# Optimization experiments

Hardware: AMD Instinct MI355X
Metric: run time of the kernel (lower is better)

The kernel has to match this reference:

```python
import jax, jax.numpy as jnp
import numpy as np

B, S, D = 4, 1024, 1024
H = 16
DH = D // H           # 64
ROT = 64              # rotary_emb_dim (full head dim)
NEG_INF = -10000.0
ROPE_BASE = 10000.0


def _rope_tables(seqlen, rot_dim, dtype=jnp.float32):
    inv_freq = 1.0 / (ROPE_BASE ** (jnp.arange(0, rot_dim, 2, dtype=jnp.float32) / rot_dim))
    t = jnp.arange(seqlen, dtype=jnp.float32)
    freqs = jnp.einsum('s,f->sf', t, inv_freq)  # (S, rot_dim//2)
    return jnp.cos(freqs).astype(dtype), jnp.sin(freqs).astype(dtype)


def _apply_rotary(x, cos, sin):
    # x: (B, S, H, DH); GPT-NeoX (non-interleaved) rotary over first ROT dims
    half = ROT // 2
    x_rot, x_pass = x[..., :ROT], x[..., ROT:]
    x1, x2 = x_rot[..., :half], x_rot[..., half:]
    c = cos[None, :, None, :]
    s = sin[None, :, None, :]
    rot = jnp.concatenate([x1 * c - x2 * s, x2 * c + x1 * s], axis=-1)
    return jnp.concatenate([rot, x_pass], axis=-1) if x_pass.shape[-1] else rot


def setup_inputs() -> dict:
    key = jax.random.key(0)
    ks = jax.random.split(key, 5)
    sc_in = 1.0 / np.sqrt(D)
    return {
        'x': jax.random.normal(ks[0], (B, S, D), jnp.float32),
        'Wqkv': jax.random.normal(ks[1], (3 * D, D), jnp.float32) * sc_in,
        'bqkv': jax.random.normal(ks[2], (3 * D,), jnp.float32) * 0.01,
        'Wout': jax.random.normal(ks[3], (D, D), jnp.float32) * sc_in,
        'bout': jax.random.normal(ks[4], (D,), jnp.float32) * 0.01,
    }


def reference(x, Wqkv, bqkv, Wout, bout):
    # QKV projection: (B,S,D) -> (B,S,3,H,DH)
    qkv = (jnp.einsum('bsd,ed->bse', x, Wqkv) + bqkv).reshape(B, S, 3, H, DH)
    q, k, v = qkv[:, :, 0], qkv[:, :, 1], qkv[:, :, 2]
    cos, sin = _rope_tables(S, ROT, q.dtype)
    q = _apply_rotary(q, cos, sin)
    k = _apply_rotary(k, cos, sin)
    scale = 1.0 / np.sqrt(DH)
    scores = jnp.einsum('bthd,bshd->bhts', q, k * scale)  # (B,H,S,S)
    causal_mask = jnp.triu(jnp.full((S, S), NEG_INF, dtype=scores.dtype), 1)
    scores = scores + causal_mask
    attn = jax.nn.softmax(scores, axis=-1)
    out = jnp.einsum('bhts,bshd->bthd', attn, v).reshape(B, S, D)
    return jnp.einsum('bsd,ed->bse', out, Wout) + bout
```

## Files before the change

kernel.cpp:

```cpp
#include <hip/hip_runtime.h>

#define B_ 4
#define S_ 1024
#define D_ 1024
#define H_ 16
#define DH_ 64

typedef unsigned short u16;
typedef __attribute__((ext_vector_type(8))) short bf16x8;
typedef __attribute__((ext_vector_type(4))) float f32x4;

__device__ __forceinline__ float bf2f(u16 h){
  union { unsigned u; float f; } x; x.u = ((unsigned)h) << 16; return x.f;
}
__device__ __forceinline__ u16 f2bf(float f){
  union { float f; unsigned u; } x; x.f = f;
  unsigned u = x.u;
  return (u16)((u + 0x7fffu + ((u >> 16) & 1u)) >> 16);
}

__device__ __forceinline__ void gload16(const u16* g, u16* l){
  __builtin_amdgcn_global_load_lds(
      (const __attribute__((address_space(1))) unsigned int*)g,
      (__attribute__((address_space(3))) unsigned int*)l, 16, 0, 0);
}

__global__ __launch_bounds__(256) void cast3(
    const float* __restrict__ a, u16* __restrict__ oa, int na,
    const float* __restrict__ b, u16* __restrict__ ob, int nb,
    const float* __restrict__ c, u16* __restrict__ oc){
  int i = (blockIdx.x * 256 + threadIdx.x) * 4;
  const float* src; u16* dst;
  if (i < na){ src = a + i; dst = oa + i; }
  else if (i < na + nb){ src = b + (i - na); dst = ob + (i - na); }
  else { src = c + (i - na - nb); dst = oc + (i - na - nb); }
  float4 v = *(const float4*)src;
  union { u16 s[4]; uint2 u; } o;
  o.s[0] = f2bf(v.x); o.s[1] = f2bf(v.y); o.s[2] = f2bf(v.z); o.s[3] = f2bf(v.w);
  *(uint2*)dst = o.u;
}

__global__ __launch_bounds__(256) void rope_tab(float2* __restrict__ tab){
  int idx = blockIdx.x * 256 + threadIdx.x;
  int s = idx >> 5, i = idx & 31;
  float invf = powf(10000.0f, -(float)i * (1.0f / 32.0f));
  float sn, cs;
  sincosf((float)s * invf, &sn, &cs);
  tab[idx] = make_float2(cs, sn);
}

__global__ __launch_bounds__(512, 2) void gemm_qkv8(const u16* __restrict__ A,
    const u16* __restrict__ Bm, const float* __restrict__ bias,
    const float2* __restrict__ tab,
    u16* __restrict__ qb, u16* __restrict__ kb, u16* __restrict__ vtb){
  __shared__ u16 As_[2][2][128*64];
  __shared__ u16 Bs_[2][2][128*64];
  const int K = 1024;
  const int tid = threadIdx.x;
  const int lane = tid & 63, wid = tid >> 6;
  const int wr = wid >> 2, wc = wid & 3;
  const int lo = lane & 15, g = lane >> 4;

  const int bid = blockIdx.x;
  const int swz = (bid & 7) * 24 + (bid >> 3);
  const int bx = swz & 15, by = swz >> 4;
  const int m0 = bx * 256, n0 = by * 256;

  f32x4 acc[8][4];
  #pragma unroll
  for (int i = 0; i < 8; ++i)
    #pragma unroll
    for (int j = 0; j < 4; ++j) acc[i][j] = (f32x4){0.f, 0.f, 0.f, 0.f};

  auto stage_p0 = [&](int b, int kt){
    const u16* ga = A + (size_t)m0 * K + kt * 64;
    const u16* gb = Bm + (size_t)n0 * K + kt * 64;
    {
      int c = tid;
      int r = c >> 3;
      int colbs = ((c & 7) * 16) ^ ((r & 7) << 4);
      int src = r * K + (colbs >> 1);
      gload16(ga + src,         &As_[b][0][c * 8]);
      gload16(ga + 128*K + src, &As_[b][1][c * 8]);
      gload16(gb + src,         &Bs_[b][0][c * 8]);
      gload16(gb + 128*K + src, &Bs_[b][1][c * 8]);
    }
    {
      int c = tid + 512;
      int r = c >> 3;
      int colbs = ((c & 7) * 16) ^ ((r & 7) << 4);
      int src = r * K + (colbs >> 1);
      gload16(gb + src,         &Bs_[b][0][c * 8]);
      gload16(gb + 128*K + src, &Bs_[b][1][c * 8]);
    }
  };
  auto stage_p1 = [&](int b, int kt){
    const u16* ga = A + (size_t)m0 * K + kt * 64;
    int c = tid + 512;
    int r = c >> 3;
    int colbs = ((c & 7) * 16) ^ ((r & 7) << 4);
    int src = r * K + (colbs >> 1);
    gload16(ga + src,         &As_[b][0][c * 8]);
    gload16(ga + 128*K + src, &As_[b][1][c * 8]);
  };

  auto rdA = [&](int b, int qm, int fm, int ks) -> bf16x8 {
    int row = qm*64 + fm*16 + lo;
    int byte = row*128 + ((ks*64 + g*16) ^ ((lo & 7) << 4));
    return *(const bf16x8*)(&As_[b][wr][byte >> 1]);
  };
  auto rdB = [&](int b, int fn, int ks) -> bf16x8 {
    int row = (wc & 1)*64 + fn*16 + lo;
    int byte = row*128 + ((ks*64 + g*16) ^ ((lo & 7) << 4));
    return *(const bf16x8*)(&Bs_[b][wc >> 1][byte >> 1]);
  };

  auto ktile = [&](int b, int stage_t){
    bf16x8 a[8], bq[8];
    #pragma unroll
    for (int fm = 0; fm < 4; ++fm)
      #pragma unroll
      for (int ks = 0; ks < 2; ++ks) a[fm*2+ks] = rdA(b, 0, fm, ks);
    #pragma unroll
    for (int fn = 0; fn < 4; ++fn)
      #pragma unroll
      for (int ks = 0; ks < 2; ++ks) bq[fn*2+ks] = rdB(b, fn, ks);
    __builtin_amdgcn_s_setprio(1);
    #pragma unroll
    for (int fm = 0; fm < 4; ++fm)
      #pragma unroll
      for (int fn = 0; fn < 2; ++fn)
        #pragma unroll
        for (int ks = 0; ks < 2; ++ks)
          acc[fm][fn] = __builtin_amdgcn_mfma_f32_16x16x32_bf16(a[fm*2+ks], bq[fn*2+ks], acc[fm][fn], 0, 0, 0);
    __builtin_amdgcn_s_setprio(0);
    asm volatile("s_waitcnt lgkmcnt(0)" ::: "memory");
    __builtin_amdgcn_sched_barrier(0);
    __builtin_amdgcn_s_barrier();
    __builtin_amdgcn_sched_barrier(0);
    if (stage_t >= 0) stage_p0(b, stage_t);
    __builtin_amdgcn_s_setprio(1);
    #pragma unroll
    for (int fm = 0; fm < 4; ++fm)
      #pragma unroll
      for (int fn = 0; fn < 2; ++fn)
        #pragma unroll
        for (int ks = 0; ks < 2; ++ks)
          acc[fm][2+fn] = __builtin_amdgcn_mfma_f32_16x16x32_bf16(a[fm*2+ks], bq[(2+fn)*2+ks], acc[fm][2+fn], 0, 0, 0);
    __builtin_amdgcn_s_setprio(0);
    #pragma unroll
    for (int fm = 0; fm < 4; ++fm)
      #pragma unroll
      for (int ks = 0; ks < 2; ++ks) a[fm*2+ks] = rdA(b, 1, fm, ks);
    __builtin_amdgcn_s_setprio(1);
    #pragma unroll
    for (int fm = 0; fm < 4; ++fm)
      #pragma unroll
      for (int fn = 0; fn < 2; ++fn)
        #pragma unroll
        for (int ks = 0; ks < 2; ++ks)
          acc[4+fm][fn] = __builtin_amdgcn_mfma_f32_16x16x32_bf16(a[fm*2+ks], bq[fn*2+ks], acc[4+fm][fn], 0, 0, 0);
    __builtin_amdgcn_s_setprio(0);
    asm volatile("s_waitcnt lgkmcnt(0)" ::: "memory");
    __builtin_amdgcn_sched_barrier(0);
    __builtin_amdgcn_s_barrier();
    __builtin_amdgcn_sched_barrier(0);
    if (stage_t >= 0) stage_p1(b, stage_t);
    __builtin_amdgcn_s_setprio(1);
    #pragma unroll
    for (int fm = 0; fm < 4; ++fm)
      #pragma unroll
      for (int fn = 0; fn < 2; ++fn)
        #pragma unroll
        for (int ks = 0; ks < 2; ++ks)
          acc[4+fm][2+fn] = __builtin_amdgcn_mfma_f32_16x16x32_bf16(a[fm*2+ks], bq[(2+fn)*2+ks], acc[4+fm][2+fn], 0, 0, 0);
    __builtin_amdgcn_s_setprio(0);
  };

  stage_p0(0, 0); stage_p1(0, 0);
  stage_p0(1, 1); stage_p1(1, 1);
  for (int t = 0; t < 14; ++t){
    asm volatile("s_waitcnt vmcnt(8)" ::: "memory");
    __builtin_amdgcn_s_barrier();
    __builtin_amdgcn_sched_barrier(0);
    ktile(t & 1, t + 2);
  }
  asm volatile("s_waitcnt vmcnt(8)" ::: "memory");
  __builtin_amdgcn_s_barrier();
  __builtin_amdgcn_sched_barrier(0);
  ktile(0, -1);
  asm volatile("s_waitcnt vmcnt(0)" ::: "memory");
  __builtin_amdgcn_s_barrier();
  __builtin_amdgcn_sched_barrier(0);
  ktile(1, -1);

  const int ty = by >> 2;
  const int h  = (by & 3) * 4 + wc;
  float bv[4];
  #pragma unroll
  for (int fn = 0; fn < 4; ++fn) bv[fn] = bias[n0 + wc*64 + fn*16 + lo];

  if (ty < 2){
    u16* dst = (ty == 0) ? qb : kb;
    #pragma unroll
    for (int fm = 0; fm < 8; ++fm){
      #pragma unroll
      for (int j = 0; j < 4; ++j){
        int row = m0 + wr*128 + fm*16 + g*4 + j;
        int bb = row >> 10, s = row & 1023;
        size_t obase = (((size_t)(bb * H_ + h)) * S_ + s) * DH_;
        #pragma unroll
        for (int fn = 0; fn < 2; ++fn){
          int i = fn*16 + lo;
          float2 t2 = tab[s*32 + i];
          float v1 = acc[fm][fn][j] + bv[fn];
          float v2 = acc[fm][fn+2][j] + bv[fn+2];
          dst[obase + i]      = f2bf(v1 * t2.x - v2 * t2.y);
          dst[obase + i + 32] = f2bf(v2 * t2.x + v1 * t2.y);
        }
      }
    }
  } else {
    __syncthreads();
    u16* wbase = (wid < 4) ? ((u16*)As_ + wid * 8192)
                           : ((u16*)Bs_ + (wid - 4) * 8192);
    #pragma unroll
    for (int fm = 0; fm < 8; ++fm)
      #pragma unroll
      for (int fn = 0; fn < 4; ++fn){
        int d = fn*16 + lo;
        #pragma unroll
        for (int j = 0; j < 4; ++j){
          int sl = fm*16 + g*4 + j;
          int sx = sl ^ ((d & 7) << 4);
          wbase[d*128 + sx] = f2bf(acc[fm][fn][j] + bv[fn]);
        }
      }
    const int rowblk = m0 + wr*128;
    const int bb = rowblk >> 10;
    const int sbase = rowblk & 1023;
    #pragma unroll
    for (int pass = 0; pass < 16; ++pass){
      int d = pass*4 + g;
      int sc = lo * 8;
      int sx = sc ^ ((d & 7) << 4);
      bf16x8 v = *(const bf16x8*)(&wbase[d*128 + sx]);
      *(bf16x8*)(vtb + (((size_t)(bb * H_ + h)) * DH_ + d) * S_ + sbase + sc) = v;
    }
  }
}

template<int OUT_BF16>
__global__ __launch_bounds__(256) void gemm_bt(const u16* __restrict__ A,
    const u16* __restrict__ Bm, const float* __restrict__ bias,
    void* __restrict__ Cout, int M, int N, int K){
  __shared__ u16 As[2][128*32];
  __shared__ u16 Bs[2][128*32];
  const int tid = threadIdx.x;
  const int lane = tid & 63;
  const int w = tid >> 6;
  const int wr = w >> 1, wc = w & 1;
  const int lo = lane & 15, g = lane >> 4;
  const int m0 = blockIdx.x * 128, n0 = blockIdx.y * 128;

  f32x4 acc[4][4];
  #pragma unroll
  for (int i = 0; i < 4; ++i)
    #pragma unroll
    for (int j = 0; j < 4; ++j) acc[i][j] = (f32x4){0.f, 0.f, 0.f, 0.f};

  const int nt = K >> 5;

  auto stage = [&](int buf, int kt){
    const u16* ga = A + (size_t)m0 * K + kt * 32;
    const u16* gb = Bm + (size_t)n0 * K + kt * 32;
    #pragma unroll
    for (int it = 0; it < 2; ++it){
      int chunk = tid + it * 256;
      int row = chunk >> 2;
      int c0 = (chunk & 3) * 8;
      gload16(ga + (size_t)row * K + c0, &As[buf][chunk * 8]);
      gload16(gb + (size_t)row * K + c0, &Bs[buf][chunk * 8]);
    }
  };

  stage(0, 0);
  __syncthreads();
  int buf = 0;
  for (int kt = 0; kt < nt; ++kt){
    if (kt + 1 < nt) stage(buf ^ 1, kt + 1);
    bf16x8 af[4], bfr[4];
    #pragma unroll
    for (int mi = 0; mi < 4; ++mi)
      af[mi] = *(const bf16x8*)(&As[buf][(wr*64 + mi*16 + lo)*32 + g*8]);
    #pragma unroll
    for (int ni = 0; ni < 4; ++ni)
      bfr[ni] = *(const bf16x8*)(&Bs[buf][(wc*64 + ni*16 + lo)*32 + g*8]);
    #pragma unroll
    for (int mi = 0; mi < 4; ++mi)
      #pragma unroll
      for (int ni = 0; ni < 4; ++ni)
        acc[mi][ni] = __builtin_amdgcn_mfma_f32_16x16x32_bf16(af[mi], bfr[ni], acc[mi][ni], 0, 0, 0);
    __syncthreads();
    buf ^= 1;
  }

  #pragma unroll
  for (int mi = 0; mi < 4; ++mi){
    int row = m0 + wr*64 + mi*16 + g*4;
    #pragma unroll
    for (int ni = 0; ni < 4; ++ni){
      int col = n0 + wc*64 + ni*16 + lo;
      float bvs = bias[col];
      #pragma unroll
      for (int j = 0; j < 4; ++j){
        float v = acc[mi][ni][j] + bvs;
        if (OUT_BF16) ((u16*)Cout)[(size_t)(row + j) * N + col] = f2bf(v);
        else          ((float*)Cout)[(size_t)(row + j) * N + col] = v;
      }
    }
  }
}

__global__ __launch_bounds__(256) void attn_fwd(const u16* __restrict__ qb,
    const u16* __restrict__ kb, const u16* __restrict__ vtb,
    u16* __restrict__ ctx){
  const int bh = blockIdx.x;
  const int qt = 15 - blockIdx.y;
  const int b = bh >> 4, h = bh & 15;
  const int tid = threadIdx.x;
  const int lane = tid & 63, w = tid >> 6;
  const int lo = lane & 15, g = lane >> 4;

  __shared__ u16 Kl[2][64*64];
  __shared__ u16 Vl[2][64*64];
  __shared__ u16 Plds[4][16][72];

  auto stage = [&](int buf, int kt){
    const u16* ksrc = kb  + ((size_t)bh * S_ + kt*64) * DH_;
    const u16* vsrc = vtb + (size_t)bh * DH_ * S_ + kt*64;
    #pragma unroll
    for (int it = 0; it < 2; ++it){
      int c = tid + it * 256;
      int row = c >> 3;
      int colbs = ((c & 7) * 16) ^ ((row & 7) << 4);
      gload16(ksrc + (size_t)row * DH_ + (colbs >> 1), &Kl[buf][c * 8]);
      gload16(vsrc + (size_t)row * S_  + (colbs >> 1), &Vl[buf][c * 8]);
    }
  };

  stage(0, 0);

  bf16x8 qf[2];
  {
    const u16* qa = qb + ((size_t)bh * S_ + qt*64 + w*16 + lo) * DH_ + g*8;
    qf[0] = *(const bf16x8*)(qa);  qf[1] = *(const bf16x8*)(qa + 32);
  }

  float m_run[4], l_run[4];
  f32x4 O[4];
  #pragma unroll
  for (int j = 0; j < 4; ++j){ m_run[j] = -1e30f; l_run[j] = 0.f; }
  #pragma unroll
  for (int c = 0; c < 4; ++c) O[c] = (f32x4){0.f,0.f,0.f,0.f};

  int buf = 0;

  auto computeTile = [&](bool diag){
    f32x4 sacc[4];
    #pragma unroll
    for (int c = 0; c < 4; ++c) sacc[c] = (f32x4){0.f,0.f,0.f,0.f};
    __builtin_amdgcn_s_setprio(1);
    #pragma unroll
    for (int cf = 0; cf < 4; ++cf){
      int r = cf*16 + lo;
      #pragma unroll
      for (int ks = 0; ks < 2; ++ks){
        int byteoff = r*128 + ((ks*64 + g*16) ^ ((lo & 7) << 4));
        bf16x8 kf = *(const bf16x8*)(&Kl[buf][byteoff >> 1]);
        sacc[cf] = __builtin_amdgcn_mfma_f32_16x16x32_bf16(qf[ks], kf, sacc[cf], 0, 0, 0);
      }
    }
    __builtin_amdgcn_s_setprio(0);
    #pragma unroll
    for (int cf = 0; cf < 4; ++cf){
      #pragma unroll
      for (int j = 0; j < 4; ++j){
        float sv = sacc[cf][j] * 0.125f;
        if (diag){
          int kj = cf*16 + lo;
          int qr = w*16 + g*4 + j;
          if (kj > qr) sv -= 10000.f;
        }
        sacc[cf][j] = sv;
      }
    }
    float rowmax[4];
    #pragma unroll
    for (int j = 0; j < 4; ++j){
      float v = fmaxf(fmaxf(sacc[0][j], sacc[1][j]), fmaxf(sacc[2][j], sacc[3][j]));
      v = fmaxf(v, __shfl_xor(v, 1));
      v = fmaxf(v, __shfl_xor(v, 2));
      v = fmaxf(v, __shfl_xor(v, 4));
      v = fmaxf(v, __shfl_xor(v, 8));
      rowmax[j] = v;
    }
    float need = fmaxf(fmaxf(rowmax[0]-m_run[0], rowmax[1]-m_run[1]),
                       fmaxf(rowmax[2]-m_run[2], rowmax[3]-m_run[3]));
    float rsum[4] = {0.f,0.f,0.f,0.f};
    if (__all(need <= 8.0f)){
      #pragma unroll
      for (int cf = 0; cf < 4; ++cf)
        #pragma unroll
        for (int j = 0; j < 4; ++j){
          float pv = __expf(sacc[cf][j] - m_run[j]);
          sacc[cf][j] = pv;
          rsum[j] += pv;
        }
      #pragma unroll
      for (int j = 0; j < 4; ++j){
        float v = rsum[j];
        v += __shfl_xor(v, 1);
        v += __shfl_xor(v, 2);
        v += __shfl_xor(v, 4);
        v += __shfl_xor(v, 8);
        l_run[j] += v;
      }
    } else {
      float alpha[4];
      #pragma unroll
      for (int j = 0; j < 4; ++j){
        float mnew = fmaxf(m_run[j], rowmax[j]);
        alpha[j] = __expf(m_run[j] - mnew);
        m_run[j] = mnew;
      }
      #pragma unroll
      for (int cf = 0; cf < 4; ++cf)
        #pragma unroll
        for (int j = 0; j < 4; ++j){
          float pv = __expf(sacc[cf][j] - m_run[j]);
          sacc[cf][j] = pv;
          rsum[j] += pv;
        }
      #pragma unroll
      for (int j = 0; j < 4; ++j){
        float v = rsum[j];
        v += __shfl_xor(v, 1);
        v += __shfl_xor(v, 2);
        v += __shfl_xor(v, 4);
        v += __shfl_xor(v, 8);
        l_run[j] = l_run[j] * alpha[j] + v;
      }
      #pragma unroll
      for (int c = 0; c < 4; ++c)
        #pragma unroll
        for (int j = 0; j < 4; ++j) O[c][j] *= alpha[j];
    }

    #pragma unroll
    for (int cf = 0; cf < 4; ++cf){
      #pragma unroll
      for (int jp = 0; jp < 2; ++jp){
        unsigned pk;
        asm("v_cvt_pk_bf16_f32 %0, %1, %2"
            : "=v"(pk) : "v"(sacc[cf][jp*2]), "v"(sacc[cf][jp*2+1]));
        Plds[w][g*4 + jp*2][cf*16 + lo]     = (u16)(pk & 0xffffu);
        Plds[w][g*4 + jp*2 + 1][cf*16 + lo] = (u16)(pk >> 16);
      }
    }

    __builtin_amdgcn_s_setprio(1);
    #pragma unroll
    for (int ks = 0; ks < 2; ++ks){
      bf16x8 pf = *(const bf16x8*)(&Plds[w][lo][ks*32 + g*8]);
      #pragma unroll
      for (int ocf = 0; ocf < 4; ++ocf){
        int r = ocf*16 + lo;
        int byteoff = r*128 + ((ks*64 + g*16) ^ ((lo & 7) << 4));
        bf16x8 vf = *(const bf16x8*)(&Vl[buf][byteoff >> 1]);
        O[ocf] = __builtin_amdgcn_mfma_f32_16x16x32_bf16(pf, vf, O[ocf], 0, 0, 0);
      }
    }
    __builtin_amdgcn_s_setprio(0);
  };

  for (int kt = 0; kt <= qt; ++kt){
    __syncthreads();
    if (kt < qt) stage(buf ^ 1, kt + 1);
    computeTile(kt == qt);
    buf ^= 1;
  }

  float inv[4];
  #pragma unroll
  for (int j = 0; j < 4; ++j) inv[j] = 1.0f / l_run[j];
  #pragma unroll
  for (int ocf = 0; ocf < 4; ++ocf){
    #pragma unroll
    for (int j = 0; j < 4; ++j){
      int d = ocf*16 + lo;
      int qi = qt*64 + w*16 + g*4 + j;
      ctx[((size_t)(b * S_ + qi)) * D_ + h * DH_ + d] = f2bf(O[ocf][j] * inv[j]);
    }
  }
}

extern "C" void kernel_launch(void* const* d_in, const int* in_sizes, int n_in,
                              void* d_out, int out_size, void* d_ws, size_t ws_size,
                              hipStream_t stream){
  (void)in_sizes; (void)n_in; (void)out_size; (void)ws_size;
  const float* x    = (const float*)d_in[0];
  const float* Wqkv = (const float*)d_in[1];
  const float* bqkv = (const float*)d_in[2];
  const float* Wout = (const float*)d_in[3];
  const float* bout = (const float*)d_in[4];
  float* out = (float*)d_out;

  char* p = (char*)d_ws;
  u16* x_bf    = (u16*)p; p += (size_t)4096*1024*2;
  u16* wqkv_bf = (u16*)p; p += (size_t)3072*1024*2;
  u16* wout_bf = (u16*)p; p += (size_t)1024*1024*2;
  u16* q_bf    = (u16*)p; p += (size_t)4096*1024*2;
  u16* k_bf    = (u16*)p; p += (size_t)4096*1024*2;
  u16* vt_bf   = (u16*)p; p += (size_t)4096*1024*2;
  u16* ctx_bf  = (u16*)p; p += (size_t)4096*1024*2;
  float2* tab  = (float2*)p; p += (size_t)1024*32*8;

  const int na = 4096*1024, nb = 3072*1024;
  cast3<<<8192, 256, 0, stream>>>(x, x_bf, na, Wqkv, wqkv_bf, nb, Wout, wout_bf);
  rope_tab<<<128, 256, 0, stream>>>(tab);

  gemm_qkv8<<<192, 512, 0, stream>>>(x_bf, wqkv_bf, bqkv, tab, q_bf, k_bf, vt_bf);

  attn_fwd<<<dim3(64, 16), 256, 0, stream>>>(q_bf, k_bf, vt_bf, ctx_bf);

  gemm_bt<0><<<dim3(32, 8), 256, 0, stream>>>(ctx_bf, wout_bf, bout, out, 4096, 1024, 1024);
}
```

Baseline: 109.3 us.

## Shrink QKV GEMM tiles, pipeline out-proj GEMM, fuse rope table, swizzle P LDS

The QKV projection GEMM changes from 256x256 tiles with 512 threads to 128x128 tiles with 256 threads, three blocks per CU and a K step of 32, giving 768 blocks instead of 192. The output projection gets the same swizzled LDS layout, block-index swizzle and split-barrier double-buffered pipeline. The rope table computation is folded into the cast kernel to save a launch, and the attention P buffer drops its padding in favour of an XOR swizzle. Smaller tiles aim to improve occupancy and CU balance but cost more global traffic per FLOP. A redundant duplicated bias load is left in the epilogue.

```diff
diff --git a/kernel.cpp b/kernel.cpp
--- a/kernel.cpp
+++ b/kernel.cpp
@@ -25,10 +25,20 @@
       (__attribute__((address_space(3))) unsigned int*)l, 16, 0, 0);
 }
 
-__global__ __launch_bounds__(256) void cast3(
+__global__ __launch_bounds__(256) void cast3tab(
     const float* __restrict__ a, u16* __restrict__ oa, int na,
     const float* __restrict__ b, u16* __restrict__ ob, int nb,
-    const float* __restrict__ c, u16* __restrict__ oc){
+    const float* __restrict__ c, u16* __restrict__ oc,
+    float2* __restrict__ tab){
+  if (blockIdx.x >= 8192){
+    int idx = (blockIdx.x - 8192) * 256 + threadIdx.x;
+    int s = idx >> 5, i = idx & 31;
+    float invf = powf(10000.0f, -(float)i * (1.0f / 32.0f));
+    float sn, cs;
+    sincosf((float)s * invf, &sn, &cs);
+    tab[idx] = make_float2(cs, sn);
+    return;
+  }
   int i = (blockIdx.x * 256 + threadIdx.x) * 4;
   const float* src; u16* dst;
   if (i < na){ src = a + i; dst = oa + i; }
@@ -40,152 +50,88 @@
   *(uint2*)dst = o.u;
 }
 
-__global__ __launch_bounds__(256) void rope_tab(float2* __restrict__ tab){
-  int idx = blockIdx.x * 256 + threadIdx.x;
-  int s = idx >> 5, i = idx & 31;
-  float invf = powf(10000.0f, -(float)i * (1.0f / 32.0f));
-  float sn, cs;
-  sincosf((float)s * invf, &sn, &cs);
-  tab[idx] = make_float2(cs, sn);
-}
-
-__global__ __launch_bounds__(512, 2) void gemm_qkv8(const u16* __restrict__ A,
+__global__ __launch_bounds__(256, 3) void gemm_qkv(const u16* __restrict__ A,
     const u16* __restrict__ Bm, const float* __restrict__ bias,
     const float2* __restrict__ tab,
     u16* __restrict__ qb, u16* __restrict__ kb, u16* __restrict__ vtb){
-  __shared__ u16 As_[2][2][128*64];
-  __shared__ u16 Bs_[2][2][128*64];
+  __shared__ u16 As_[2][128*32];
+  __shared__ u16 Bs_[2][128*32];
   const int K = 1024;
   const int tid = threadIdx.x;
-  const int lane = tid & 63, wid = tid >> 6;
-  const int wr = wid >> 2, wc = wid & 3;
+  const int lane = tid & 63, w = tid >> 6;
+  const int wr = w >> 1, wc = w & 1;
   const int lo = lane & 15, g = lane >> 4;
 
   const int bid = blockIdx.x;
-  const int swz = (bid & 7) * 24 + (bid >> 3);
-  const int bx = swz & 15, by = swz >> 4;
-  const int m0 = bx * 256, n0 = by * 256;
-
-  f32x4 acc[8][4];
-  #pragma unroll
-  for (int i = 0; i < 8; ++i)
+  const int swz = (bid & 7) * 96 + (bid >> 3);
+  const int mx = swz & 31, ny = swz >> 5;
+  const int m0 = mx * 128, n0 = ny * 128;
+
+  f32x4 acc[4][4];
+  #pragma unroll
+  for (int i = 0; i < 4; ++i)
     #pragma unroll
     for (int j = 0; j < 4; ++j) acc[i][j] = (f32x4){0.f, 0.f, 0.f, 0.f};
 
-  auto stage_p0 = [&](int b, int kt){
-    const u16* ga = A + (size_t)m0 * K + kt * 64;
-    const u16* gb = Bm + (size_t)n0 * K + kt * 64;
-    {
-      int c = tid;
-      int r = c >> 3;
-      int colbs = ((c & 7) * 16) ^ ((r & 7) << 4);
-      int src = r * K + (colbs >> 1);
-      gload16(ga + src,         &As_[b][0][c * 8]);
-      gload16(ga + 128*K + src, &As_[b][1][c * 8]);
-      gload16(gb + src,         &Bs_[b][0][c * 8]);
-      gload16(gb + 128*K + src, &Bs_[b][1][c * 8]);
-    }
-    {
-      int c = tid + 512;
-      int r = c >> 3;
-      int colbs = ((c & 7) * 16) ^ ((r & 7) << 4);
-      int src = r * K + (colbs >> 1);
-      gload16(gb + src,         &Bs_[b][0][c * 8]);
-      gload16(gb + 128*K + src, &Bs_[b][1][c * 8]);
-    }
-  };
-  auto stage_p1 = [&](int b, int kt){
-    const u16* ga = A + (size_t)m0 * K + kt * 64;
-    int c = tid + 512;
-    int r = c >> 3;
-    int colbs = ((c & 7) * 16) ^ ((r & 7) << 4);
-    int src = r * K + (colbs >> 1);
-    gload16(ga + src,         &As_[b][0][c * 8]);
-    gload16(ga + 128*K + src, &As_[b][1][c * 8]);
-  };
-
-  auto rdA = [&](int b, int qm, int fm, int ks) -> bf16x8 {
-    int row = qm*64 + fm*16 + lo;
-    int byte = row*128 + ((ks*64 + g*16) ^ ((lo & 7) << 4));
-    return *(const bf16x8*)(&As_[b][wr][byte >> 1]);
-  };
-  auto rdB = [&](int b, int fn, int ks) -> bf16x8 {
-    int row = (wc & 1)*64 + fn*16 + lo;
-    int byte = row*128 + ((ks*64 + g*16) ^ ((lo & 7) << 4));
-    return *(const bf16x8*)(&Bs_[b][wc >> 1][byte >> 1]);
+  auto stage = [&](int b, int kt){
+    const u16* ga = A + (size_t)m0 * K + kt * 32;
+    const u16* gb = Bm + (size_t)n0 * K + kt * 32;
+    #pragma unroll
+    for (int it = 0; it < 2; ++it){
+      int c = tid + it * 256;
+      int r = c >> 2;
+      int cbs = ((c & 3) * 16) ^ ((r & 3) << 4);
+      gload16(ga + r * K + (cbs >> 1), &As_[b][c * 8]);
+      gload16(gb + r * K + (cbs >> 1), &Bs_[b][c * 8]);
+    }
+  };
+
+  auto rdA = [&](int b, int fm) -> bf16x8 {
+    int row = wr*64 + fm*16 + lo;
+    int byte = row*64 + ((g*16) ^ ((row & 3) << 4));
+    return *(const bf16x8*)(&As_[b][byte >> 1]);
+  };
+  auto rdB = [&](int b, int fn) -> bf16x8 {
+    int row = wc*64 + fn*16 + lo;
+    int byte = row*64 + ((g*16) ^ ((row & 3) << 4));
+    return *(const bf16x8*)(&Bs_[b][byte >> 1]);
   };
 
   auto ktile = [&](int b, int stage_t){
-    bf16x8 a[8], bq[8];
-    #pragma unroll
-    for (int fm = 0; fm < 4; ++fm)
-      #pragma unroll
-      for (int ks = 0; ks < 2; ++ks) a[fm*2+ks] = rdA(b, 0, fm, ks);
-    #pragma unroll
-    for (int fn = 0; fn < 4; ++fn)
-      #pragma unroll
-      for (int ks = 0; ks < 2; ++ks) bq[fn*2+ks] = rdB(b, fn, ks);
-    __builtin_amdgcn_s_setprio(1);
-    #pragma unroll
-    for (int fm = 0; fm < 4; ++fm)
-      #pragma unroll
-      for (int fn = 0; fn < 2; ++fn)
-        #pragma unroll
-        for (int ks = 0; ks < 2; ++ks)
-          acc[fm][fn] = __builtin_amdgcn_mfma_f32_16x16x32_bf16(a[fm*2+ks], bq[fn*2+ks], acc[fm][fn], 0, 0, 0);
-    __builtin_amdgcn_s_setprio(0);
+    bf16x8 af[4], bf[4];
+    #pragma unroll
+    for (int fm = 0; fm < 4; ++fm) af[fm] = rdA(b, fm);
+    #pragma unroll
+    for (int fn = 0; fn < 4; ++fn) bf[fn] = rdB(b, fn);
     asm volatile("s_waitcnt lgkmcnt(0)" ::: "memory");
     __builtin_amdgcn_sched_barrier(0);
+    __builtin_amdgcn_s_setprio(1);
+    #pragma unroll
+    for (int fm = 0; fm < 4; ++fm)
+      #pragma unroll
+      for (int fn = 0; fn < 2; ++fn)
+        acc[fm][fn] = __builtin_amdgcn_mfma_f32_16x16x32_bf16(af[fm], bf[fn], acc[fm][fn], 0, 0, 0);
+    __builtin_amdgcn_s_setprio(0);
     __builtin_amdgcn_s_barrier();
-    __builtin_amdgcn_sched_barrier(0);
-    if (stage_t >= 0) stage_p0(b, stage_t);
+    if (stage_t >= 0) stage(b, stage_t);
     __builtin_amdgcn_s_setprio(1);
     #pragma unroll
     for (int fm = 0; fm < 4; ++fm)
       #pragma unroll
-      for (int fn = 0; fn < 2; ++fn)
-        #pragma unroll
-        for (int ks = 0; ks < 2; ++ks)
-          acc[fm][2+fn] = __builtin_amdgcn_mfma_f32_16x16x32_bf16(a[fm*2+ks], bq[(2+fn)*2+ks], acc[fm][2+fn], 0, 0, 0);
+      for (int fn = 2; fn < 4; ++fn)
+        acc[fm][fn] = __builtin_amdgcn_mfma_f32_16x16x32_bf16(af[fm], bf[fn], acc[fm][fn], 0, 0, 0);
     __builtin_amdgcn_s_setprio(0);
-    #pragma unroll
-    for (int fm = 0; fm < 4; ++fm)
-      #pragma unroll
-      for (int ks = 0; ks < 2; ++ks) a[fm*2+ks] = rdA(b, 1, fm, ks);
-    __builtin_amdgcn_s_setprio(1);
-    #pragma unroll
-    for (int fm = 0; fm < 4; ++fm)
-      #pragma unroll
-      for (int fn = 0; fn < 2; ++fn)
-        #pragma unroll
-        for (int ks = 0; ks < 2; ++ks)
-          acc[4+fm][fn] = __builtin_amdgcn_mfma_f32_16x16x32_bf16(a[fm*2+ks], bq[fn*2+ks], acc[4+fm][fn], 0, 0, 0);
-    __builtin_amdgcn_s_setprio(0);
-    asm volatile("s_waitcnt lgkmcnt(0)" ::: "memory");
-    __builtin_amdgcn_sched_barrier(0);
-    __builtin_amdgcn_s_barrier();
-    __builtin_amdgcn_sched_barrier(0);
-    if (stage_t >= 0) stage_p1(b, stage_t);
-    __builtin_amdgcn_s_setprio(1);
-    #pragma unroll
-    for (int fm = 0; fm < 4; ++fm)
-      #pragma unroll
-      for (int fn = 0; fn < 2; ++fn)
-        #pragma unroll
-        for (int ks = 0; ks < 2; ++ks)
-          acc[4+fm][2+fn] = __builtin_amdgcn_mfma_f32_16x16x32_bf16(a[fm*2+ks], bq[(2+fn)*2+ks], acc[4+fm][2+fn], 0, 0, 0);
-    __builtin_amdgcn_s_setprio(0);
-  };
-
-  stage_p0(0, 0); stage_p1(0, 0);
-  stage_p0(1, 1); stage_p1(1, 1);
-  for (int t = 0; t < 14; ++t){
-    asm volatile("s_waitcnt vmcnt(8)" ::: "memory");
+  };
+
+  stage(0, 0);
+  stage(1, 1);
+  for (int t = 0; t < 30; ++t){
+    asm volatile("s_waitcnt vmcnt(4)" ::: "memory");
     __builtin_amdgcn_s_barrier();
     __builtin_amdgcn_sched_barrier(0);
     ktile(t & 1, t + 2);
   }
-  asm volatile("s_waitcnt vmcnt(8)" ::: "memory");
+  asm volatile("s_waitcnt vmcnt(4)" ::: "memory");
   __builtin_amdgcn_s_barrier();
   __builtin_amdgcn_sched_barrier(0);
   ktile(0, -1);
@@ -194,19 +140,22 @@
   __builtin_amdgcn_sched_barrier(0);
   ktile(1, -1);
 
-  const int ty = by >> 2;
-  const int h  = (by & 3) * 4 + wc;
+  const int gcb = n0 + wc*64;
+  const int ty = gcb >> 10;
+  const int h  = (gcb >> 6) & 15;
   float bv[4];
   #pragma unroll
-  for (int fn = 0; fn < 4; ++fn) bv[fn] = bias[n0 + wc*64 + fn*16 + lo];
+  for (int fn = 0; fn < 4; ++fn) bv[fn] = bias[gcb + fn*16 + lo - wc*64 + wc*64];
+  #pragma unroll
+  for (int fn = 0; fn < 4; ++fn) bv[fn] = bias[gcb + fn*16 + lo];
 
   if (ty < 2){
     u16* dst = (ty == 0) ? qb : kb;
     #pragma unroll
-    for (int fm = 0; fm < 8; ++fm){
+    for (int fm = 0; fm < 4; ++fm){
       #pragma unroll
       for (int j = 0; j < 4; ++j){
-        int row = m0 + wr*128 + fm*16 + g*4 + j;
+        int row = m0 + wr*64 + fm*16 + g*4 + j;
         int bb = row >> 10, s = row & 1023;
         size_t obase = (((size_t)(bb * H_ + h)) * S_ + s) * DH_;
         #pragma unroll
@@ -222,46 +171,46 @@
     }
   } else {
     __syncthreads();
-    u16* wbase = (wid < 4) ? ((u16*)As_ + wid * 8192)
-                           : ((u16*)Bs_ + (wid - 4) * 8192);
-    #pragma unroll
-    for (int fm = 0; fm < 8; ++fm)
+    u16* wbase = (w < 2) ? ((u16*)As_ + w * 4096) : ((u16*)Bs_ + (w - 2) * 4096);
+    #pragma unroll
+    for (int fm = 0; fm < 4; ++fm)
       #pragma unroll
       for (int fn = 0; fn < 4; ++fn){
         int d = fn*16 + lo;
         #pragma unroll
         for (int j = 0; j < 4; ++j){
           int sl = fm*16 + g*4 + j;
-          int sx = sl ^ ((d & 7) << 4);
-          wbase[d*128 + sx] = f2bf(acc[fm][fn][j] + bv[fn]);
+          wbase[d*64 + (sl ^ ((d & 7) << 3))] = f2bf(acc[fm][fn][j] + bv[fn]);
         }
       }
-    const int rowblk = m0 + wr*128;
+    const int rowblk = m0 + wr*64;
     const int bb = rowblk >> 10;
     const int sbase = rowblk & 1023;
     #pragma unroll
     for (int pass = 0; pass < 16; ++pass){
       int d = pass*4 + g;
-      int sc = lo * 8;
-      int sx = sc ^ ((d & 7) << 4);
-      bf16x8 v = *(const bf16x8*)(&wbase[d*128 + sx]);
-      *(bf16x8*)(vtb + (((size_t)(bb * H_ + h)) * DH_ + d) * S_ + sbase + sc) = v;
-    }
-  }
-}
-
-template<int OUT_BF16>
-__global__ __launch_bounds__(256) void gemm_bt(const u16* __restrict__ A,
+      int sc = lo * 4;
+      uint2 v = *(const uint2*)(&wbase[d*64 + (sc ^ ((d & 7) << 3))]);
+      *(uint2*)(vtb + (((size_t)(bb * H_ + h)) * DH_ + d) * S_ + sbase + sc) = v;
+    }
+  }
+}
+
+__global__ __launch_bounds__(256, 3) void gemm_out(const u16* __restrict__ A,
     const u16* __restrict__ Bm, const float* __restrict__ bias,
-    void* __restrict__ Cout, int M, int N, int K){
-  __shared__ u16 As[2][128*32];
-  __shared__ u16 Bs[2][128*32];
+    float* __restrict__ Cout){
+  __shared__ u16 As_[2][128*32];
+  __shared__ u16 Bs_[2][128*32];
+  const int K = 1024;
   const int tid = threadIdx.x;
-  const int lane = tid & 63;
-  const int w = tid >> 6;
+  const int lane = tid & 63, w = tid >> 6;
   const int wr = w >> 1, wc = w & 1;
   const int lo = lane & 15, g = lane >> 4;
-  const int m0 = blockIdx.x * 128, n0 = blockIdx.y * 128;
+
+  const int bid = blockIdx.x;
+  const int swz = (bid & 7) * 32 + (bid >> 3);
+  const int mx = swz & 31, ny = swz >> 5;
+  const int m0 = mx * 128, n0 = ny * 128;
 
   f32x4 acc[4][4];
   #pragma unroll
@@ -269,54 +218,82 @@
     #pragma unroll
     for (int j = 0; j < 4; ++j) acc[i][j] = (f32x4){0.f, 0.f, 0.f, 0.f};
 
-  const int nt = K >> 5;
-
-  auto stage = [&](int buf, int kt){
+  auto stage = [&](int b, int kt){
     const u16* ga = A + (size_t)m0 * K + kt * 32;
     const u16* gb = Bm + (size_t)n0 * K + kt * 32;
     #pragma unroll
     for (int it = 0; it < 2; ++it){
-      int chunk = tid + it * 256;
-      int row = chunk >> 2;
-      int c0 = (chunk & 3) * 8;
-      gload16(ga + (size_t)row * K + c0, &As[buf][chunk * 8]);
-      gload16(gb + (size_t)row * K + c0, &Bs[buf][chunk * 8]);
-    }
+      int c = tid + it * 256;
+      int r = c >> 2;
+      int cbs = ((c & 3) * 16) ^ ((r & 3) << 4);
+      gload16(ga + r * K + (cbs >> 1), &As_[b][c * 8]);
+      gload16(gb + r * K + (cbs >> 1), &Bs_[b][c * 8]);
+    }
+  };
+
+  auto rdA = [&](int b, int fm) -> bf16x8 {
+    int row = wr*64 + fm*16 + lo;
+    int byte = row*64 + ((g*16) ^ ((row & 3) << 4));
+    return *(const bf16x8*)(&As_[b][byte >> 1]);
+  };
+  auto rdB = [&](int b, int fn) -> bf16x8 {
+    int row = wc*64 + fn*16 + lo;
+    int byte = row*64 + ((g*16) ^ ((row & 3) << 4));
+    return *(const bf16x8*)(&Bs_[b][byte >> 1]);
+  };
+
+  auto ktile = [&](int b, int stage_t){
+    bf16x8 af[4], bf[4];
+    #pragma unroll
+    for (int fm = 0; fm < 4; ++fm) af[fm] = rdA(b, fm);
+    #pragma unroll
+    for (int fn = 0; fn < 4; ++fn) bf[fn] = rdB(b, fn);
+    asm volatile("s_waitcnt lgkmcnt(0)" ::: "memory");
+    __builtin_amdgcn_sched_barrier(0);
+    __builtin_amdgcn_s_setprio(1);
+    #pragma unroll
+    for (int fm = 0; fm < 4; ++fm)
+      #pragma unroll
+      for (int fn = 0; fn < 2; ++fn)
+        acc[fm][fn] = __builtin_amdgcn_mfma_f32_16x16x32_bf16(af[fm], bf[fn], acc[fm][fn], 0, 0, 0);
+    __builtin_amdgcn_s_setprio(0);
+    __builtin_amdgcn_s_barrier();
+    if (stage_t >= 0) stage(b, stage_t);
+    __builtin_amdgcn_s_setprio(1);
+    #pragma unroll
+    for (int fm = 0; fm < 4; ++fm)
+      #pragma unroll
+      for (int fn = 2; fn < 4; ++fn)
+        acc[fm][fn] = __builtin_amdgcn_mfma_f32_16x16x32_bf16(af[fm], bf[fn], acc[fm][fn], 0, 0, 0);
+    __builtin_amdgcn_s_setprio(0);
   };
 
   stage(0, 0);
-  __syncthreads();
-  int buf = 0;
-  for (int kt = 0; kt < nt; ++kt){
-    if (kt + 1 < nt) stage(buf ^ 1, kt + 1);
-    bf16x8 af[4], bfr[4];
-    #pragma unroll
-    for (int mi = 0; mi < 4; ++mi)
-      af[mi] = *(const bf16x8*)(&As[buf][(wr*64 + mi*16 + lo)*32 + g*8]);
-    #pragma unroll
-    for (int ni = 0; ni < 4; ++ni)
-      bfr[ni] = *(const bf16x8*)(&Bs[buf][(wc*64 + ni*16 + lo)*32 + g*8]);
-    #pragma unroll
-    for (int mi = 0; mi < 4; ++mi)
-      #pragma unroll
-      for (int ni = 0; ni < 4; ++ni)
-        acc[mi][ni] = __builtin_amdgcn_mfma_f32_16x16x32_bf16(af[mi], bfr[ni], acc[mi][ni], 0, 0, 0);
-    __syncthreads();
-    buf ^= 1;
-  }
-
-  #pragma unroll
-  for (int mi = 0; mi < 4; ++mi){
-    int row = m0 + wr*64 + mi*16 + g*4;
-    #pragma unroll
-    for (int ni = 0; ni < 4; ++ni){
-      int col = n0 + wc*64 + ni*16 + lo;
-      float bvs = bias[col];
-      #pragma unroll
-      for (int j = 0; j < 4; ++j){
-        float v = acc[mi][ni][j] + bvs;
-        if (OUT_BF16) ((u16*)Cout)[(size_t)(row + j) * N + col] = f2bf(v);
-        else          ((float*)Cout)[(size_t)(row + j) * N + col] = v;
+  stage(1, 1);
+  for (int t = 0; t < 30; ++t){
+    asm volatile("s_waitcnt vmcnt(4)" ::: "memory");
+    __builtin_amdgcn_s_barrier();
+    __builtin_amdgcn_sched_barrier(0);
+    ktile(t & 1, t + 2);
+  }
+  asm volatile("s_waitcnt vmcnt(4)" ::: "memory");
+  __builtin_amdgcn_s_barrier();
+  __builtin_amdgcn_sched_barrier(0);
+  ktile(0, -1);
+  asm volatile("s_waitcnt vmcnt(0)" ::: "memory");
+  __builtin_amdgcn_s_barrier();
+  __builtin_amdgcn_sched_barrier(0);
+  ktile(1, -1);
+
+  #pragma unroll
+  for (int fm = 0; fm < 4; ++fm){
+    #pragma unroll
+    for (int j = 0; j < 4; ++j){
+      int row = m0 + wr*64 + fm*16 + g*4 + j;
+      #pragma unroll
+      for (int fn = 0; fn < 4; ++fn){
+        int col = n0 + wc*64 + fn*16 + lo;
+        Cout[(size_t)row * 1024 + col] = acc[fm][fn][j] + bias[col];
       }
     }
   }
@@ -334,7 +311,7 @@
 
   __shared__ u16 Kl[2][64*64];
   __shared__ u16 Vl[2][64*64];
-  __shared__ u16 Plds[4][16][72];
+  __shared__ u16 Plds[4][16][64];
 
   auto stage = [&](int buf, int kt){
     const u16* ksrc = kb  + ((size_t)bh * S_ + kt*64) * DH_;
@@ -464,15 +441,16 @@
         unsigned pk;
         asm("v_cvt_pk_bf16_f32 %0, %1, %2"
             : "=v"(pk) : "v"(sacc[cf][jp*2]), "v"(sacc[cf][jp*2+1]));
-        Plds[w][g*4 + jp*2][cf*16 + lo]     = (u16)(pk & 0xffffu);
-        Plds[w][g*4 + jp*2 + 1][cf*16 + lo] = (u16)(pk >> 16);
+        int r1 = g*4 + jp*2, r2 = r1 + 1;
+        Plds[w][r1][(cf*16 + lo) ^ ((r1 & 7) << 3)] = (u16)(pk & 0xffffu);
+        Plds[w][r2][(cf*16 + lo) ^ ((r2 & 7) << 3)] = (u16)(pk >> 16);
       }
     }
 
     __builtin_amdgcn_s_setprio(1);
     #pragma unroll
     for (int ks = 0; ks < 2; ++ks){
-      bf16x8 pf = *(const bf16x8*)(&Plds[w][lo][ks*32 + g*8]);
+      bf16x8 pf = *(const bf16x8*)(&Plds[w][lo][(ks*32 + g*8) ^ ((lo & 7) << 3)]);
       #pragma unroll
       for (int ocf = 0; ocf < 4; ++ocf){
         int r = ocf*16 + lo;
@@ -527,12 +505,11 @@
   float2* tab  = (float2*)p; p += (size_t)1024*32*8;
 
   const int na = 4096*1024, nb = 3072*1024;
-  cast3<<<8192, 256, 0, stream>>>(x, x_bf, na, Wqkv, wqkv_bf, nb, Wout, wout_bf);
-  rope_tab<<<128, 256, 0, stream>>>(tab);
-
-  gemm_qkv8<<<192, 512, 0, stream>>>(x_bf, wqkv_bf, bqkv, tab, q_bf, k_bf, vt_bf);
+  cast3tab<<<8320, 256, 0, stream>>>(x, x_bf, na, Wqkv, wqkv_bf, nb, Wout, wout_bf, tab);
+
+  gemm_qkv<<<768, 256, 0, stream>>>(x_bf, wqkv_bf, bqkv, tab, q_bf, k_bf, vt_bf);
 
   attn_fwd<<<dim3(64, 16), 256, 0, stream>>>(q_bf, k_bf, vt_bf, ctx_bf);
 
-  gemm_bt<0><<<dim3(32, 8), 256, 0, stream>>>(ctx_bf, wout_bf, bout, out, 4096, 1024, 1024);
-}
+  gemm_out<<<256, 256, 0, stream>>>(ctx_bf, wout_bf, bout, out);
+}
```

Result: faster. 102.1 us (-6.6%).
